# Kernel optimization log

Measured on AMD Instinct MI355X. Metric: run time of the kernel, lower is better.

The kernel has to match this reference:

```python
import jax, jax.numpy as jnp
import numpy as np

N_HEADS = 16
D_EMBED = 1024
D_HEAD = D_EMBED // N_HEADS
CAUSAL = False


def setup_inputs() -> dict:
    key = jax.random.key(0)
    k1, k2, k3, k4, k5 = jax.random.split(key, 5)
    B, S, D = 4, 2048, D_EMBED
    scale = 1.0 / np.sqrt(D)
    return {
        "x": jax.random.normal(k1, (B, S, D), dtype=jnp.float32),
        "w_in": jax.random.normal(k2, (D, 3 * D), dtype=jnp.float32) * scale,
        "b_in": jax.random.normal(k3, (3 * D,), dtype=jnp.float32) * 0.02,
        "w_out": jax.random.normal(k4, (D, D), dtype=jnp.float32) * scale,
        "b_out": jax.random.normal(k5, (D,), dtype=jnp.float32) * 0.02,
    }


def reference(x, w_in, b_in, w_out, b_out):
    B, S, D = x.shape
    qkv = jnp.einsum("bsd,de->bse", x, w_in) + b_in  # [B,S,3D]
    q, k, v = jnp.split(qkv, 3, axis=-1)
    # split heads -> [B,H,S,Dh]
    def sh(t):
        return t.reshape(B, S, N_HEADS, D_HEAD).transpose(0, 2, 1, 3)
    q, k, v = sh(q), sh(k), sh(v)
    weight = jnp.einsum("bhsd,bhtd->bhst", q, k)  # [B,H,S,S]
    if CAUSAL:
        mask = jnp.triu(jnp.ones((S, S), dtype=bool), k=1)
        weight = jnp.where(mask, -jnp.inf, weight)
    weight = weight / np.sqrt(D_HEAD)
    weight = jax.nn.softmax(weight, axis=-1)
    out = jnp.einsum("bhst,bhtd->bhsd", weight, v)
    out = out.transpose(0, 2, 1, 3).reshape(B, S, D)
    return jnp.einsum("bsd,de->bse", out, w_out) + b_out
```

## Files before the change

kernel.cpp:

```cpp
#include <hip/hip_runtime.h>
#include <hip/hip_bf16.h>

typedef unsigned short u16;
typedef __attribute__((ext_vector_type(8))) short bf16x8;
typedef __attribute__((ext_vector_type(4))) float f32x4;
typedef __attribute__((ext_vector_type(16))) float f32x16;

#define QSCALE 0.180336880f

#define DEV static __device__ __forceinline__

DEV u16 f2bf(float f) {
  union { float f; unsigned u; } v; v.f = f;
  unsigned r = v.u + 0x7fffu + ((v.u >> 16) & 1u);
  return (u16)(r >> 16);
}

DEV unsigned pk2(float a, float b) {
  union { __hip_bfloat162 h; unsigned u; } c;
  c.h = __float22bfloat162_rn(make_float2(a, b));
  return c.u;
}

DEV void gll16(void* lds, const void* g) {
  __builtin_amdgcn_global_load_lds(
      (const __attribute__((address_space(1))) unsigned int*)g,
      (__attribute__((address_space(3))) unsigned int*)lds, 16, 0, 0);
}

__global__ __launch_bounds__(256) void cvt_f32_to_bf16(const float* __restrict__ in,
                                                       u16* __restrict__ out, int n4) {
  int i = blockIdx.x * blockDim.x + threadIdx.x;
  int stride = gridDim.x * blockDim.x;
  for (; i < n4; i += stride) {
    float4 f = ((const float4*)in)[i];
    ushort4 u;
    u.x = f2bf(f.x); u.y = f2bf(f.y); u.z = f2bf(f.z); u.w = f2bf(f.w);
    ((ushort4*)out)[i] = u;
  }
}

__global__ __launch_bounds__(256) void transpose_cvt(const float* __restrict__ W,
                                                     u16* __restrict__ Wt,
                                                     int K, int N, int sn, float sval) {
  __shared__ u16 t[64][65];
  const int k0 = blockIdx.x * 64, n0 = blockIdx.y * 64;
  const int tid = threadIdx.x;
  const int rr = tid >> 4;
  const int cc = (tid & 15) * 4;
  const float scl = (n0 < sn) ? sval : 1.0f;
#pragma unroll
  for (int i = 0; i < 4; ++i) {
    const int row = rr * 4 + i;
    float4 f = *(const float4*)&W[(size_t)(k0 + row) * N + n0 + cc];
    t[row][cc + 0] = f2bf(f.x * scl);
    t[row][cc + 1] = f2bf(f.y * scl);
    t[row][cc + 2] = f2bf(f.z * scl);
    t[row][cc + 3] = f2bf(f.w * scl);
  }
  __syncthreads();
#pragma unroll
  for (int i = 0; i < 4; ++i) {
    const int n = rr * 4 + i;
    ushort4 u;
    u.x = t[cc + 0][n]; u.y = t[cc + 1][n]; u.z = t[cc + 2][n]; u.w = t[cc + 3][n];
    *(ushort4*)&Wt[(size_t)(n0 + n) * K + k0 + cc] = u;
  }
}

__global__ __launch_bounds__(256) void transpose_v(const u16* __restrict__ qkv,
                                                   u16* __restrict__ vT) {
  __shared__ u16 t[64][72];
  const int bh = blockIdx.y;
  const int b = bh >> 4, h = bh & 15;
  const int t0 = blockIdx.x * 64;
  const int tid = threadIdx.x;
  const int row = tid >> 2;
  const int cg = (tid & 3) * 16;
  const size_t src = (size_t)b * 2048 * 3072 + (size_t)(t0 + row) * 3072 + 2048 + h * 64 + cg;
  bf16x8 v0 = *(const bf16x8*)&qkv[src];
  bf16x8 v1 = *(const bf16x8*)&qkv[src + 8];
#pragma unroll
  for (int i = 0; i < 8; ++i) { t[row][cg + i] = (u16)v0[i]; t[row][cg + 8 + i] = (u16)v1[i]; }
  __syncthreads();
  const int d = tid >> 2;
  const int tg = (tid & 3) * 16;
  bf16x8 o0, o1;
#pragma unroll
  for (int i = 0; i < 8; ++i) { o0[i] = (short)t[tg + i][d]; o1[i] = (short)t[tg + 8 + i][d]; }
  u16* dst = &vT[((size_t)bh * 64 + d) * 2048 + t0 + tg];
  *(bf16x8*)dst = o0;
  *(bf16x8*)(dst + 8) = o1;
}

template<bool OUT_BF16>
__global__ __launch_bounds__(256) void gemm_bf16(const u16* __restrict__ A,
                                                 const u16* __restrict__ Bt,
                                                 const float* __restrict__ bias,
                                                 void* __restrict__ Cout,
                                                 int M, int N, int K, int qn,
                                                 u16* __restrict__ vTout, int vn0) {
  __shared__ __align__(16) u16 As[128][64];
  __shared__ __align__(16) u16 Bs[128][64];
  const int tid = threadIdx.x;
  const int wave = tid >> 6, lane = tid & 63;
  const int g = lane >> 4, lr = lane & 15;
  const int bm = blockIdx.x * 128, bn = blockIdx.y * 128;
  const int wm = (wave >> 1) * 64, wn = (wave & 1) * 64;
  f32x4 acc[4][4] = {};
  for (int kt = 0; kt < K; kt += 64) {
    __syncthreads();
#pragma unroll
    for (int j = 0; j < 4; ++j) {
      int chunk = wave * 4 + j;
      int e = chunk * 512 + lane * 8;
      int r = e >> 6, c = e & 63;
      gll16((u16*)As + chunk * 512, &A[(size_t)(bm + r) * K + kt + c]);
      gll16((u16*)Bs + chunk * 512, &Bt[(size_t)(bn + r) * K + kt + c]);
    }
    __syncthreads();
#pragma unroll
    for (int kk = 0; kk < 64; kk += 32) {
      bf16x8 af[4], bfr[4];
#pragma unroll
      for (int m = 0; m < 4; ++m)
        af[m] = *(const bf16x8*)&As[wm + m * 16 + lr][kk + g * 8];
#pragma unroll
      for (int n = 0; n < 4; ++n)
        bfr[n] = *(const bf16x8*)&Bs[wn + n * 16 + lr][kk + g * 8];
#pragma unroll
      for (int m = 0; m < 4; ++m)
#pragma unroll
        for (int n = 0; n < 4; ++n)
          acc[m][n] = __builtin_amdgcn_mfma_f32_16x16x32_bf16(af[m], bfr[n], acc[m][n], 0, 0, 0);
    }
  }
#pragma unroll
  for (int m = 0; m < 4; ++m) {
#pragma unroll
    for (int n = 0; n < 4; ++n) {
      const int col = bn + wn + n * 16 + lr;
      float bv = bias ? bias[col] : 0.f;
      if (col < qn) bv *= QSCALE;
      if (vTout != nullptr && col >= vn0) {
        const int hc = col - vn0;
#pragma unroll
        for (int r = 0; r < 4; ++r) {
          const int row = bm + wm + m * 16 + g * 4 + r;
          const size_t idx = (((size_t)(row >> 11) * 16 + (hc >> 6)) * 64 + (hc & 63)) * 2048
                             + (row & 2047);
          vTout[idx] = f2bf(acc[m][n][r] + bv);
        }
      } else {
#pragma unroll
        for (int r = 0; r < 4; ++r) {
          const int row = bm + wm + m * 16 + g * 4 + r;
          float v = acc[m][n][r] + bv;
          if (OUT_BF16) ((u16*)Cout)[(size_t)row * N + col] = f2bf(v);
          else          ((float*)Cout)[(size_t)row * N + col] = v;
        }
      }
    }
  }
}


#define ATTN_BODY(BUF, ISSUE, VM)                                                 \
  {                                                                               \
    if (ISSUE) {                                                                  \
      gll16((u16*)Ks[((BUF) + 2) & 3] + wave * 512, gk); gk += 32 * 3072;         \
      gll16((u16*)Vs[((BUF) + 2) & 3] + wave * 512, gv); gv += 32;                \
    }                                                                             \
    asm volatile("s_waitcnt vmcnt(" #VM ")" ::: "memory");                        \
    __builtin_amdgcn_s_barrier();                                                 \
    const char* kb = (const char*)Ks[(BUF)];                                      \
    const char* vb = (const char*)Vs[(BUF)];                                      \
    f32x16 s = {};                                                                \
    __builtin_amdgcn_s_setprio(1);                                                \
    _Pragma("unroll")                                                             \
    for (int kk = 0; kk < 4; ++kk) {                                              \
      bf16x8 kf = *(const bf16x8*)(kb + koff[kk]);                                \
      s = __builtin_amdgcn_mfma_f32_32x32x16_bf16(kf, qf[kk], s, 0, 0, 0);        \
    }                                                                             \
    __builtin_amdgcn_s_setprio(0);                                                \
    float pr[16];                                                                 \
    _Pragma("unroll")                                                             \
    for (int r = 0; r < 16; ++r) pr[r] = __builtin_amdgcn_exp2f(s[r]);            \
    lsum += ((pr[0] + pr[1]) + (pr[2] + pr[3])) + ((pr[4] + pr[5]) + (pr[6] + pr[7])) \
          + ((pr[8] + pr[9]) + (pr[10] + pr[11])) + ((pr[12] + pr[13]) + (pr[14] + pr[15])); \
    union { unsigned u[4]; bf16x8 v; } pa0, pa1;                                  \
    {                                                                             \
      unsigned X0 = pk2(pr[0], pr[1]), X1 = pk2(pr[2], pr[3]);                    \
      unsigned Y0 = pk2(pr[4], pr[5]), Y1 = pk2(pr[6], pr[7]);                    \
      asm volatile("v_permlane32_swap_b32 %0, %1" : "+v"(X0), "+v"(Y0));          \
      asm volatile("v_permlane32_swap_b32 %0, %1" : "+v"(X1), "+v"(Y1));          \
      pa0.u[0] = X0; pa0.u[1] = X1; pa0.u[2] = Y0; pa0.u[3] = Y1;                 \
      unsigned Z0 = pk2(pr[8], pr[9]), Z1 = pk2(pr[10], pr[11]);                  \
      unsigned W0 = pk2(pr[12], pr[13]), W1 = pk2(pr[14], pr[15]);                \
      asm volatile("v_permlane32_swap_b32 %0, %1" : "+v"(Z0), "+v"(W0));          \
      asm volatile("v_permlane32_swap_b32 %0, %1" : "+v"(Z1), "+v"(W1));          \
      pa1.u[0] = Z0; pa1.u[1] = Z1; pa1.u[2] = W0; pa1.u[3] = W1;                 \
    }                                                                             \
    __builtin_amdgcn_s_setprio(1);                                                \
    {                                                                             \
      bf16x8 vf00 = *(const bf16x8*)(vb + voff[0][0]);                            \
      bf16x8 vf10 = *(const bf16x8*)(vb + voff[1][0]);                            \
      o0 = __builtin_amdgcn_mfma_f32_32x32x16_bf16(pa0.v, vf00, o0, 0, 0, 0);     \
      o1 = __builtin_amdgcn_mfma_f32_32x32x16_bf16(pa0.v, vf10, o1, 0, 0, 0);     \
      bf16x8 vf01 = *(const bf16x8*)(vb + voff[0][1]);                            \
      bf16x8 vf11 = *(const bf16x8*)(vb + voff[1][1]);                            \
      o0 = __builtin_amdgcn_mfma_f32_32x32x16_bf16(pa1.v, vf01, o0, 0, 0, 0);     \
      o1 = __builtin_amdgcn_mfma_f32_32x32x16_bf16(pa1.v, vf11, o1, 0, 0, 0);     \
    }                                                                             \
    __builtin_amdgcn_s_setprio(0);                                                \
  }

__global__ __launch_bounds__(256, 4) void attn_kernel(const u16* __restrict__ qkv,
                                                      const u16* __restrict__ vT,
                                                      u16* __restrict__ out) {
  __shared__ __align__(16) u16 Ks[4][2048];
  __shared__ __align__(16) u16 Vs[4][2048];
  const int tid = threadIdx.x;
  const int wave = tid >> 6, lane = tid & 63;
  const int hi = lane >> 5, l31 = lane & 31;
  const int id = blockIdx.x;
  const int bh = ((id >> 3) & 7) * 8 + (id & 7);
  const int b = bh >> 4, h = bh & 15;
  const int q0 = (id >> 6) * 128;
  const size_t base = (size_t)b * 2048 * 3072;
  const u16* kg = qkv + base + 1024 + h * 64;
  const u16* vg = vT + (size_t)bh * 64 * 2048;

  const int qrow = q0 + wave * 32 + l31;
  bf16x8 qf[4];
#pragma unroll
  for (int kk = 0; kk < 4; ++kk)
    qf[kk] = *(const bf16x8*)&qkv[base + (size_t)qrow * 3072 + h * 64 + kk * 16 + hi * 8];

  int koff[4];
#pragma unroll
  for (int kk = 0; kk < 4; ++kk)
    koff[kk] = (kk * 2 + hi) * 512 + l31 * 16;
  int voff[2][2];
#pragma unroll
  for (int dt = 0; dt < 2; ++dt)
#pragma unroll
    for (int kp = 0; kp < 2; ++kp)
      voff[dt][kp] = (dt * 4 + kp * 2 + hi) * 512 + l31 * 16;

  const u16* gk = kg + (size_t)l31 * 3072 + wave * 16 + hi * 8;
  const u16* gv = vg + (size_t)((wave >> 1) * 32 + l31) * 2048 + (wave & 1) * 16 + hi * 8;

  f32x16 o0 = {}, o1 = {};
  float lsum = 0.f;

  gll16((u16*)Ks[0] + wave * 512, gk); gk += 32 * 3072;
  gll16((u16*)Vs[0] + wave * 512, gv); gv += 32;
  gll16((u16*)Ks[1] + wave * 512, gk); gk += 32 * 3072;
  gll16((u16*)Vs[1] + wave * 512, gv); gv += 32;

  for (int it4 = 0; it4 < 15; ++it4) {
    ATTN_BODY(0, true, 4)
    ATTN_BODY(1, true, 4)
    ATTN_BODY(2, true, 4)
    ATTN_BODY(3, true, 4)
  }
  ATTN_BODY(0, true, 4)
  ATTN_BODY(1, true, 4)
  ATTN_BODY(2, false, 2)
  ATTN_BODY(3, false, 0)

  float lt = lsum + __shfl_xor(lsum, 32);
  const size_t orow0 = (size_t)b * 2048 + q0 + wave * 32;
#pragma unroll
  for (int r = 0; r < 16; ++r) {
    const int crow = (r & 3) + 8 * (r >> 2) + 4 * hi;
    const float li = __shfl(lt, crow);
    u16* orow = out + (orow0 + crow) * 1024 + h * 64 + l31;
    orow[0]  = f2bf(o0[r] / li);
    orow[32] = f2bf(o1[r] / li);
  }
}

extern "C" void kernel_launch(void* const* d_in, const int* in_sizes, int n_in,
                              void* d_out, int out_size, void* d_ws, size_t ws_size,
                              hipStream_t stream) {
  (void)in_sizes; (void)n_in; (void)out_size;
  const float* x     = (const float*)d_in[0];
  const float* w_in  = (const float*)d_in[1];
  const float* b_in  = (const float*)d_in[2];
  const float* w_out = (const float*)d_in[3];
  const float* b_out = (const float*)d_in[4];
  float* out = (float*)d_out;

  char* ws = (char*)d_ws;
  u16* Xbf   = (u16*)ws; ws += (size_t)8192 * 1024 * 2;
  u16* WinT  = (u16*)ws; ws += (size_t)3072 * 1024 * 2;
  u16* WoutT = (u16*)ws; ws += (size_t)1024 * 1024 * 2;
  u16* qkv   = (u16*)ws; ws += (size_t)8192 * 3072 * 2;
  u16* attno = (u16*)ws; ws += (size_t)8192 * 1024 * 2;
  u16* vTsep = (u16*)ws;

  const size_t fused_need = 92274688ull + 16777216ull;
  const bool fused = (ws_size >= fused_need);
  u16* vT = fused ? vTsep : Xbf;

  cvt_f32_to_bf16<<<2048, 256, 0, stream>>>(x, Xbf, 8192 * 1024 / 4);
  transpose_cvt<<<dim3(16, 48), 256, 0, stream>>>(w_in, WinT, 1024, 3072, 1024, QSCALE);
  transpose_cvt<<<dim3(16, 16), 256, 0, stream>>>(w_out, WoutT, 1024, 1024, 0, 1.0f);
  if (fused) {
    gemm_bf16<true ><<<dim3(64, 24), 256, 0, stream>>>(Xbf, WinT, b_in, qkv,
                                                       8192, 3072, 1024, 1024, vT, 2048);
  } else {
    gemm_bf16<true ><<<dim3(64, 24), 256, 0, stream>>>(Xbf, WinT, b_in, qkv,
                                                       8192, 3072, 1024, 1024, nullptr, 1 << 30);
    transpose_v<<<dim3(32, 64), 256, 0, stream>>>(qkv, vT);
  }
  attn_kernel<<<1024, 256, 0, stream>>>(qkv, vT, attno);
  gemm_bf16<false><<<dim3(64, 8), 256, 0, stream>>>(attno, WoutT, b_out, out,
                                                    8192, 1024, 1024, 0, nullptr, 1 << 30);
}
```

Baseline: 226.6 us.

## Store V transposed inside QKV buffer, process 64-key tiles, XCD-aware GEMM tile mapping

The QKV GEMM epilogue now writes V in transposed layout into the unused V columns of the qkv buffer, so the separate vT workspace and the fallback transpose kernel go away. The attention loop moves from a 4-deep pipeline of 32-key tiles to a double-buffered loop over 64-key tiles, with two independent QK^T accumulators per step and one wait and barrier per tile. The GEMM block index is remapped so consecutive blocks on each XCD share A row tiles, aiming at better L2 reuse. In exchange, prefetch depth is shallower, register pressure per step is higher, and the V transposed-in-place indexing is intricate.

```diff
diff --git a/kernel.cpp b/kernel.cpp
--- a/kernel.cpp
+++ b/kernel.cpp
@@ -68,55 +68,33 @@
   }
 }
 
-__global__ __launch_bounds__(256) void transpose_v(const u16* __restrict__ qkv,
-                                                   u16* __restrict__ vT) {
-  __shared__ u16 t[64][72];
-  const int bh = blockIdx.y;
-  const int b = bh >> 4, h = bh & 15;
-  const int t0 = blockIdx.x * 64;
-  const int tid = threadIdx.x;
-  const int row = tid >> 2;
-  const int cg = (tid & 3) * 16;
-  const size_t src = (size_t)b * 2048 * 3072 + (size_t)(t0 + row) * 3072 + 2048 + h * 64 + cg;
-  bf16x8 v0 = *(const bf16x8*)&qkv[src];
-  bf16x8 v1 = *(const bf16x8*)&qkv[src + 8];
-#pragma unroll
-  for (int i = 0; i < 8; ++i) { t[row][cg + i] = (u16)v0[i]; t[row][cg + 8 + i] = (u16)v1[i]; }
-  __syncthreads();
-  const int d = tid >> 2;
-  const int tg = (tid & 3) * 16;
-  bf16x8 o0, o1;
-#pragma unroll
-  for (int i = 0; i < 8; ++i) { o0[i] = (short)t[tg + i][d]; o1[i] = (short)t[tg + 8 + i][d]; }
-  u16* dst = &vT[((size_t)bh * 64 + d) * 2048 + t0 + tg];
-  *(bf16x8*)dst = o0;
-  *(bf16x8*)(dst + 8) = o1;
-}
-
 template<bool OUT_BF16>
 __global__ __launch_bounds__(256) void gemm_bf16(const u16* __restrict__ A,
                                                  const u16* __restrict__ Bt,
                                                  const float* __restrict__ bias,
                                                  void* __restrict__ Cout,
-                                                 int M, int N, int K, int qn,
-                                                 u16* __restrict__ vTout, int vn0) {
+                                                 int M, int N, int K, int qn, int vn0) {
   __shared__ __align__(16) u16 As[128][64];
   __shared__ __align__(16) u16 Bs[128][64];
   const int tid = threadIdx.x;
   const int wave = tid >> 6, lane = tid & 63;
   const int g = lane >> 4, lr = lane & 15;
-  const int bm = blockIdx.x * 128, bn = blockIdx.y * 128;
+  const int lid = blockIdx.y * gridDim.x + blockIdx.x;
+  const int chunk = gridDim.x >> 3;
+  const int xcd = lid & 7, j = lid >> 3;
+  const int bm = (xcd * chunk + (j % chunk)) * 128;
+  const int bn = (j / chunk) * 128;
   const int wm = (wave >> 1) * 64, wn = (wave & 1) * 64;
   f32x4 acc[4][4] = {};
   for (int kt = 0; kt < K; kt += 64) {
     __syncthreads();
 #pragma unroll
-    for (int j = 0; j < 4; ++j) {
-      int chunk = wave * 4 + j;
-      int e = chunk * 512 + lane * 8;
+    for (int jj = 0; jj < 4; ++jj) {
+      int chnk = wave * 4 + jj;
+      int e = chnk * 512 + lane * 8;
       int r = e >> 6, c = e & 63;
-      gll16((u16*)As + chunk * 512, &A[(size_t)(bm + r) * K + kt + c]);
-      gll16((u16*)Bs + chunk * 512, &Bt[(size_t)(bn + r) * K + kt + c]);
+      gll16((u16*)As + chnk * 512, &A[(size_t)(bm + r) * K + kt + c]);
+      gll16((u16*)Bs + chnk * 512, &Bt[(size_t)(bn + r) * K + kt + c]);
     }
     __syncthreads();
 #pragma unroll
@@ -142,14 +120,15 @@
       const int col = bn + wn + n * 16 + lr;
       float bv = bias ? bias[col] : 0.f;
       if (col < qn) bv *= QSCALE;
-      if (vTout != nullptr && col >= vn0) {
+      if (col >= vn0) {
         const int hc = col - vn0;
 #pragma unroll
         for (int r = 0; r < 4; ++r) {
           const int row = bm + wm + m * 16 + g * 4 + r;
-          const size_t idx = (((size_t)(row >> 11) * 16 + (hc >> 6)) * 64 + (hc & 63)) * 2048
-                             + (row & 2047);
-          vTout[idx] = f2bf(acc[m][n][r] + bv);
+          const int t = row & 2047, bb = row >> 11;
+          const size_t idx = (size_t)bb * 6291456
+                           + ((size_t)hc * 2 + (t >> 10)) * 3072 + 2048 + (t & 1023);
+          ((u16*)Cout)[idx] = f2bf(acc[m][n][r] + bv);
         }
       } else {
 #pragma unroll
@@ -165,61 +144,94 @@
 }
 
 
-#define ATTN_BODY(BUF, ISSUE, VM)                                                 \
+#define ATTN_SUB(SOFF, PA0, PA1)                                                  \
+    f32x16 s##PA0 = {};                                                           \
+    (void)0
+
+#define ATTN_BODY(BUF, ISSUE)                                                     \
   {                                                                               \
     if (ISSUE) {                                                                  \
-      gll16((u16*)Ks[((BUF) + 2) & 3] + wave * 512, gk); gk += 32 * 3072;         \
-      gll16((u16*)Vs[((BUF) + 2) & 3] + wave * 512, gv); gv += 32;                \
-    }                                                                             \
-    asm volatile("s_waitcnt vmcnt(" #VM ")" ::: "memory");                        \
-    __builtin_amdgcn_s_barrier();                                                 \
+      gll16((u16*)Ks[(BUF) ^ 1] + wave * 512, gk);                                \
+      gll16((u16*)Ks[(BUF) ^ 1] + 2048 + wave * 512, gk + 32 * 3072);             \
+      gk += (size_t)64 * 3072;                                                    \
+      gll16((u16*)Vs[(BUF) ^ 1] + wave * 512, gv);                                \
+      gll16((u16*)Vs[(BUF) ^ 1] + 2048 + wave * 512, gv + 32);                    \
+      gv += 64;                                                                   \
+    }                                                                             \
     const char* kb = (const char*)Ks[(BUF)];                                      \
     const char* vb = (const char*)Vs[(BUF)];                                      \
-    f32x16 s = {};                                                                \
+    f32x16 sA = {}, sB = {};                                                      \
     __builtin_amdgcn_s_setprio(1);                                                \
     _Pragma("unroll")                                                             \
     for (int kk = 0; kk < 4; ++kk) {                                              \
-      bf16x8 kf = *(const bf16x8*)(kb + koff[kk]);                                \
-      s = __builtin_amdgcn_mfma_f32_32x32x16_bf16(kf, qf[kk], s, 0, 0, 0);        \
+      bf16x8 kfA = *(const bf16x8*)(kb + koff[kk]);                               \
+      bf16x8 kfB = *(const bf16x8*)(kb + 4096 + koff[kk]);                        \
+      sA = __builtin_amdgcn_mfma_f32_32x32x16_bf16(kfA, qf[kk], sA, 0, 0, 0);     \
+      sB = __builtin_amdgcn_mfma_f32_32x32x16_bf16(kfB, qf[kk], sB, 0, 0, 0);     \
     }                                                                             \
     __builtin_amdgcn_s_setprio(0);                                                \
-    float pr[16];                                                                 \
+    float prA[16], prB[16];                                                       \
     _Pragma("unroll")                                                             \
-    for (int r = 0; r < 16; ++r) pr[r] = __builtin_amdgcn_exp2f(s[r]);            \
-    lsum += ((pr[0] + pr[1]) + (pr[2] + pr[3])) + ((pr[4] + pr[5]) + (pr[6] + pr[7])) \
-          + ((pr[8] + pr[9]) + (pr[10] + pr[11])) + ((pr[12] + pr[13]) + (pr[14] + pr[15])); \
-    union { unsigned u[4]; bf16x8 v; } pa0, pa1;                                  \
+    for (int r = 0; r < 16; ++r) prA[r] = __builtin_amdgcn_exp2f(sA[r]);          \
+    _Pragma("unroll")                                                             \
+    for (int r = 0; r < 16; ++r) prB[r] = __builtin_amdgcn_exp2f(sB[r]);          \
+    lsum += (((prA[0] + prA[1]) + (prA[2] + prA[3])) + ((prA[4] + prA[5]) + (prA[6] + prA[7])))   \
+          + (((prA[8] + prA[9]) + (prA[10] + prA[11])) + ((prA[12] + prA[13]) + (prA[14] + prA[15]))); \
+    lsum += (((prB[0] + prB[1]) + (prB[2] + prB[3])) + ((prB[4] + prB[5]) + (prB[6] + prB[7])))   \
+          + (((prB[8] + prB[9]) + (prB[10] + prB[11])) + ((prB[12] + prB[13]) + (prB[14] + prB[15]))); \
+    union { unsigned u[4]; bf16x8 v; } pa0A, pa1A, pa0B, pa1B;                    \
     {                                                                             \
-      unsigned X0 = pk2(pr[0], pr[1]), X1 = pk2(pr[2], pr[3]);                    \
-      unsigned Y0 = pk2(pr[4], pr[5]), Y1 = pk2(pr[6], pr[7]);                    \
+      unsigned X0 = pk2(prA[0], prA[1]), X1 = pk2(prA[2], prA[3]);                \
+      unsigned Y0 = pk2(prA[4], prA[5]), Y1 = pk2(prA[6], prA[7]);                \
       asm volatile("v_permlane32_swap_b32 %0, %1" : "+v"(X0), "+v"(Y0));          \
       asm volatile("v_permlane32_swap_b32 %0, %1" : "+v"(X1), "+v"(Y1));          \
-      pa0.u[0] = X0; pa0.u[1] = X1; pa0.u[2] = Y0; pa0.u[3] = Y1;                 \
-      unsigned Z0 = pk2(pr[8], pr[9]), Z1 = pk2(pr[10], pr[11]);                  \
-      unsigned W0 = pk2(pr[12], pr[13]), W1 = pk2(pr[14], pr[15]);                \
+      pa0A.u[0] = X0; pa0A.u[1] = X1; pa0A.u[2] = Y0; pa0A.u[3] = Y1;             \
+      unsigned Z0 = pk2(prA[8], prA[9]), Z1 = pk2(prA[10], prA[11]);              \
+      unsigned W0 = pk2(prA[12], prA[13]), W1 = pk2(prA[14], prA[15]);            \
       asm volatile("v_permlane32_swap_b32 %0, %1" : "+v"(Z0), "+v"(W0));          \
       asm volatile("v_permlane32_swap_b32 %0, %1" : "+v"(Z1), "+v"(W1));          \
-      pa1.u[0] = Z0; pa1.u[1] = Z1; pa1.u[2] = W0; pa1.u[3] = W1;                 \
+      pa1A.u[0] = Z0; pa1A.u[1] = Z1; pa1A.u[2] = W0; pa1A.u[3] = W1;             \
+    }                                                                             \
+    {                                                                             \
+      unsigned X0 = pk2(prB[0], prB[1]), X1 = pk2(prB[2], prB[3]);                \
+      unsigned Y0 = pk2(prB[4], prB[5]), Y1 = pk2(prB[6], prB[7]);                \
+      asm volatile("v_permlane32_swap_b32 %0, %1" : "+v"(X0), "+v"(Y0));          \
+      asm volatile("v_permlane32_swap_b32 %0, %1" : "+v"(X1), "+v"(Y1));          \
+      pa0B.u[0] = X0; pa0B.u[1] = X1; pa0B.u[2] = Y0; pa0B.u[3] = Y1;             \
+      unsigned Z0 = pk2(prB[8], prB[9]), Z1 = pk2(prB[10], prB[11]);              \
+      unsigned W0 = pk2(prB[12], prB[13]), W1 = pk2(prB[14], prB[15]);            \
+      asm volatile("v_permlane32_swap_b32 %0, %1" : "+v"(Z0), "+v"(W0));          \
+      asm volatile("v_permlane32_swap_b32 %0, %1" : "+v"(Z1), "+v"(W1));          \
+      pa1B.u[0] = Z0; pa1B.u[1] = Z1; pa1B.u[2] = W0; pa1B.u[3] = W1;             \
     }                                                                             \
     __builtin_amdgcn_s_setprio(1);                                                \
     {                                                                             \
-      bf16x8 vf00 = *(const bf16x8*)(vb + voff[0][0]);                            \
-      bf16x8 vf10 = *(const bf16x8*)(vb + voff[1][0]);                            \
-      o0 = __builtin_amdgcn_mfma_f32_32x32x16_bf16(pa0.v, vf00, o0, 0, 0, 0);     \
-      o1 = __builtin_amdgcn_mfma_f32_32x32x16_bf16(pa0.v, vf10, o1, 0, 0, 0);     \
-      bf16x8 vf01 = *(const bf16x8*)(vb + voff[0][1]);                            \
-      bf16x8 vf11 = *(const bf16x8*)(vb + voff[1][1]);                            \
-      o0 = __builtin_amdgcn_mfma_f32_32x32x16_bf16(pa1.v, vf01, o0, 0, 0, 0);     \
-      o1 = __builtin_amdgcn_mfma_f32_32x32x16_bf16(pa1.v, vf11, o1, 0, 0, 0);     \
+      bf16x8 vfA00 = *(const bf16x8*)(vb + voff[0][0]);                           \
+      bf16x8 vfA10 = *(const bf16x8*)(vb + voff[1][0]);                           \
+      o0 = __builtin_amdgcn_mfma_f32_32x32x16_bf16(pa0A.v, vfA00, o0, 0, 0, 0);   \
+      o1 = __builtin_amdgcn_mfma_f32_32x32x16_bf16(pa0A.v, vfA10, o1, 0, 0, 0);   \
+      bf16x8 vfA01 = *(const bf16x8*)(vb + voff[0][1]);                           \
+      bf16x8 vfA11 = *(const bf16x8*)(vb + voff[1][1]);                           \
+      o0 = __builtin_amdgcn_mfma_f32_32x32x16_bf16(pa1A.v, vfA01, o0, 0, 0, 0);   \
+      o1 = __builtin_amdgcn_mfma_f32_32x32x16_bf16(pa1A.v, vfA11, o1, 0, 0, 0);   \
+      bf16x8 vfB00 = *(const bf16x8*)(vb + 4096 + voff[0][0]);                    \
+      bf16x8 vfB10 = *(const bf16x8*)(vb + 4096 + voff[1][0]);                    \
+      o0 = __builtin_amdgcn_mfma_f32_32x32x16_bf16(pa0B.v, vfB00, o0, 0, 0, 0);   \
+      o1 = __builtin_amdgcn_mfma_f32_32x32x16_bf16(pa0B.v, vfB10, o1, 0, 0, 0);   \
+      bf16x8 vfB01 = *(const bf16x8*)(vb + 4096 + voff[0][1]);                    \
+      bf16x8 vfB11 = *(const bf16x8*)(vb + 4096 + voff[1][1]);                    \
+      o0 = __builtin_amdgcn_mfma_f32_32x32x16_bf16(pa1B.v, vfB01, o0, 0, 0, 0);   \
+      o1 = __builtin_amdgcn_mfma_f32_32x32x16_bf16(pa1B.v, vfB11, o1, 0, 0, 0);   \
     }                                                                             \
     __builtin_amdgcn_s_setprio(0);                                                \
+    asm volatile("s_waitcnt vmcnt(0)" ::: "memory");                              \
+    __builtin_amdgcn_s_barrier();                                                 \
   }
 
 __global__ __launch_bounds__(256, 4) void attn_kernel(const u16* __restrict__ qkv,
-                                                      const u16* __restrict__ vT,
                                                       u16* __restrict__ out) {
-  __shared__ __align__(16) u16 Ks[4][2048];
-  __shared__ __align__(16) u16 Vs[4][2048];
+  __shared__ __align__(16) u16 Ks[2][4096];
+  __shared__ __align__(16) u16 Vs[2][4096];
   const int tid = threadIdx.x;
   const int wave = tid >> 6, lane = tid & 63;
   const int hi = lane >> 5, l31 = lane & 31;
@@ -229,7 +241,6 @@
   const int q0 = (id >> 6) * 128;
   const size_t base = (size_t)b * 2048 * 3072;
   const u16* kg = qkv + base + 1024 + h * 64;
-  const u16* vg = vT + (size_t)bh * 64 * 2048;
 
   const int qrow = q0 + wave * 32 + l31;
   bf16x8 qf[4];
@@ -249,26 +260,28 @@
       voff[dt][kp] = (dt * 4 + kp * 2 + hi) * 512 + l31 * 16;
 
   const u16* gk = kg + (size_t)l31 * 3072 + wave * 16 + hi * 8;
-  const u16* gv = vg + (size_t)((wave >> 1) * 32 + l31) * 2048 + (wave & 1) * 16 + hi * 8;
+  const u16* gv = qkv + base + 2048 + (size_t)(h * 64 + (wave >> 1) * 32 + l31) * 6144
+                + (wave & 1) * 16 + hi * 8;
 
   f32x16 o0 = {}, o1 = {};
   float lsum = 0.f;
 
-  gll16((u16*)Ks[0] + wave * 512, gk); gk += 32 * 3072;
-  gll16((u16*)Vs[0] + wave * 512, gv); gv += 32;
-  gll16((u16*)Ks[1] + wave * 512, gk); gk += 32 * 3072;
-  gll16((u16*)Vs[1] + wave * 512, gv); gv += 32;
-
-  for (int it4 = 0; it4 < 15; ++it4) {
-    ATTN_BODY(0, true, 4)
-    ATTN_BODY(1, true, 4)
-    ATTN_BODY(2, true, 4)
-    ATTN_BODY(3, true, 4)
-  }
-  ATTN_BODY(0, true, 4)
-  ATTN_BODY(1, true, 4)
-  ATTN_BODY(2, false, 2)
-  ATTN_BODY(3, false, 0)
+  gll16((u16*)Ks[0] + wave * 512, gk);
+  gll16((u16*)Ks[0] + 2048 + wave * 512, gk + 32 * 3072);
+  gk += (size_t)64 * 3072;
+  gll16((u16*)Vs[0] + wave * 512, gv);
+  gll16((u16*)Vs[0] + 2048 + wave * 512, gv + 32);
+  gv += 64;
+  asm volatile("s_waitcnt vmcnt(0)" ::: "memory");
+  __builtin_amdgcn_s_barrier();
+
+  for (int it = 0; it < 7; ++it) { ATTN_BODY(0, true) ATTN_BODY(1, true) }
+  ATTN_BODY(0, true)
+  gv += 2048;
+  ATTN_BODY(1, true)
+  for (int it = 0; it < 7; ++it) { ATTN_BODY(0, true) ATTN_BODY(1, true) }
+  ATTN_BODY(0, true)
+  ATTN_BODY(1, false)
 
   float lt = lsum + __shfl_xor(lsum, 32);
   const size_t orow0 = (size_t)b * 2048 + q0 + wave * 32;
@@ -285,7 +298,7 @@
 extern "C" void kernel_launch(void* const* d_in, const int* in_sizes, int n_in,
                               void* d_out, int out_size, void* d_ws, size_t ws_size,
                               hipStream_t stream) {
-  (void)in_sizes; (void)n_in; (void)out_size;
+  (void)in_sizes; (void)n_in; (void)out_size; (void)ws_size;
   const float* x     = (const float*)d_in[0];
   const float* w_in  = (const float*)d_in[1];
   const float* b_in  = (const float*)d_in[2];
@@ -298,25 +311,14 @@
   u16* WinT  = (u16*)ws; ws += (size_t)3072 * 1024 * 2;
   u16* WoutT = (u16*)ws; ws += (size_t)1024 * 1024 * 2;
   u16* qkv   = (u16*)ws; ws += (size_t)8192 * 3072 * 2;
-  u16* attno = (u16*)ws; ws += (size_t)8192 * 1024 * 2;
-  u16* vTsep = (u16*)ws;
-
-  const size_t fused_need = 92274688ull + 16777216ull;
-  const bool fused = (ws_size >= fused_need);
-  u16* vT = fused ? vTsep : Xbf;
+  u16* attno = (u16*)ws;
 
   cvt_f32_to_bf16<<<2048, 256, 0, stream>>>(x, Xbf, 8192 * 1024 / 4);
   transpose_cvt<<<dim3(16, 48), 256, 0, stream>>>(w_in, WinT, 1024, 3072, 1024, QSCALE);
   transpose_cvt<<<dim3(16, 16), 256, 0, stream>>>(w_out, WoutT, 1024, 1024, 0, 1.0f);
-  if (fused) {
-    gemm_bf16<true ><<<dim3(64, 24), 256, 0, stream>>>(Xbf, WinT, b_in, qkv,
-                                                       8192, 3072, 1024, 1024, vT, 2048);
-  } else {
-    gemm_bf16<true ><<<dim3(64, 24), 256, 0, stream>>>(Xbf, WinT, b_in, qkv,
-                                                       8192, 3072, 1024, 1024, nullptr, 1 << 30);
-    transpose_v<<<dim3(32, 64), 256, 0, stream>>>(qkv, vT);
-  }
-  attn_kernel<<<1024, 256, 0, stream>>>(qkv, vT, attno);
+  gemm_bf16<true ><<<dim3(64, 24), 256, 0, stream>>>(Xbf, WinT, b_in, qkv,
+                                                     8192, 3072, 1024, 1024, 2048);
+  attn_kernel<<<1024, 256, 0, stream>>>(qkv, attno);
   gemm_bf16<false><<<dim3(64, 8), 256, 0, stream>>>(attno, WoutT, b_out, out,
-                                                    8192, 1024, 1024, 0, nullptr, 1 << 30);
-}
+                                                    8192, 1024, 1024, 0, 1 << 30);
+}
```

After: 261.5 us. 1.15x slower.

## Double-buffer 64-key attention tiles, swizzle GEMM blocks by XCD, drop fused V transpose

Applied to the files above, without the earlier changes.

The attention loop moves from four 32-key LDS buffers with partial vmcnt waits to two 64-key buffers. Each buffer is processed as two subtiles, followed by a full wait and a barrier, which halves the number of barriers per key. The GEMM remaps block indices so that each XCD gets a contiguous band of M tiles, aiming for better L2 reuse. The fused V-transpose epilogue, with its scattered 2-byte stores, is dropped in favour of always running the separate transpose_v kernel. That adds a launch and an extra pass over V, and the full vmcnt(0) wait each iteration may expose more load latency.

```diff
diff --git a/kernel.cpp b/kernel.cpp
--- a/kernel.cpp
+++ b/kernel.cpp
@@ -26,6 +26,21 @@
   __builtin_amdgcn_global_load_lds(
       (const __attribute__((address_space(1))) unsigned int*)g,
       (__attribute__((address_space(3))) unsigned int*)lds, 16, 0, 0);
+}
+
+DEV void packP(const float* pr, bf16x8* a0, bf16x8* a1) {
+  unsigned X0 = pk2(pr[0], pr[1]), X1 = pk2(pr[2], pr[3]);
+  unsigned Y0 = pk2(pr[4], pr[5]), Y1 = pk2(pr[6], pr[7]);
+  asm volatile("v_permlane32_swap_b32 %0, %1" : "+v"(X0), "+v"(Y0));
+  asm volatile("v_permlane32_swap_b32 %0, %1" : "+v"(X1), "+v"(Y1));
+  union { unsigned u[4]; bf16x8 v; } c0, c1;
+  c0.u[0] = X0; c0.u[1] = X1; c0.u[2] = Y0; c0.u[3] = Y1;
+  unsigned Z0 = pk2(pr[8], pr[9]), Z1 = pk2(pr[10], pr[11]);
+  unsigned W0 = pk2(pr[12], pr[13]), W1 = pk2(pr[14], pr[15]);
+  asm volatile("v_permlane32_swap_b32 %0, %1" : "+v"(Z0), "+v"(W0));
+  asm volatile("v_permlane32_swap_b32 %0, %1" : "+v"(Z1), "+v"(W1));
+  c1.u[0] = Z0; c1.u[1] = Z1; c1.u[2] = W0; c1.u[3] = W1;
+  *a0 = c0.v; *a1 = c1.v;
 }
 
 __global__ __launch_bounds__(256) void cvt_f32_to_bf16(const float* __restrict__ in,
@@ -98,25 +113,28 @@
                                                  const u16* __restrict__ Bt,
                                                  const float* __restrict__ bias,
                                                  void* __restrict__ Cout,
-                                                 int M, int N, int K, int qn,
-                                                 u16* __restrict__ vTout, int vn0) {
+                                                 int M, int N, int K, int qn) {
   __shared__ __align__(16) u16 As[128][64];
   __shared__ __align__(16) u16 Bs[128][64];
   const int tid = threadIdx.x;
   const int wave = tid >> 6, lane = tid & 63;
   const int g = lane >> 4, lr = lane & 15;
-  const int bm = blockIdx.x * 128, bn = blockIdx.y * 128;
+  const int lid = blockIdx.y * gridDim.x + blockIdx.x;
+  const int chunk = gridDim.x >> 3;
+  const int xcd = lid & 7, j = lid >> 3;
+  const int bm = (xcd * chunk + (j % chunk)) * 128;
+  const int bn = (j / chunk) * 128;
   const int wm = (wave >> 1) * 64, wn = (wave & 1) * 64;
   f32x4 acc[4][4] = {};
   for (int kt = 0; kt < K; kt += 64) {
     __syncthreads();
 #pragma unroll
-    for (int j = 0; j < 4; ++j) {
-      int chunk = wave * 4 + j;
-      int e = chunk * 512 + lane * 8;
+    for (int jj = 0; jj < 4; ++jj) {
+      int chnk = wave * 4 + jj;
+      int e = chnk * 512 + lane * 8;
       int r = e >> 6, c = e & 63;
-      gll16((u16*)As + chunk * 512, &A[(size_t)(bm + r) * K + kt + c]);
-      gll16((u16*)Bs + chunk * 512, &Bt[(size_t)(bn + r) * K + kt + c]);
+      gll16((u16*)As + chnk * 512, &A[(size_t)(bm + r) * K + kt + c]);
+      gll16((u16*)Bs + chnk * 512, &Bt[(size_t)(bn + r) * K + kt + c]);
     }
     __syncthreads();
 #pragma unroll
@@ -142,84 +160,72 @@
       const int col = bn + wn + n * 16 + lr;
       float bv = bias ? bias[col] : 0.f;
       if (col < qn) bv *= QSCALE;
-      if (vTout != nullptr && col >= vn0) {
-        const int hc = col - vn0;
-#pragma unroll
-        for (int r = 0; r < 4; ++r) {
-          const int row = bm + wm + m * 16 + g * 4 + r;
-          const size_t idx = (((size_t)(row >> 11) * 16 + (hc >> 6)) * 64 + (hc & 63)) * 2048
-                             + (row & 2047);
-          vTout[idx] = f2bf(acc[m][n][r] + bv);
-        }
-      } else {
-#pragma unroll
-        for (int r = 0; r < 4; ++r) {
-          const int row = bm + wm + m * 16 + g * 4 + r;
-          float v = acc[m][n][r] + bv;
-          if (OUT_BF16) ((u16*)Cout)[(size_t)row * N + col] = f2bf(v);
-          else          ((float*)Cout)[(size_t)row * N + col] = v;
-        }
+#pragma unroll
+      for (int r = 0; r < 4; ++r) {
+        const int row = bm + wm + m * 16 + g * 4 + r;
+        float v = acc[m][n][r] + bv;
+        if (OUT_BF16) ((u16*)Cout)[(size_t)row * N + col] = f2bf(v);
+        else          ((float*)Cout)[(size_t)row * N + col] = v;
       }
     }
   }
 }
 
 
-#define ATTN_BODY(BUF, ISSUE, VM)                                                 \
+#define ATTN_SUBTILE(KB, VB)                                                      \
   {                                                                               \
-    if (ISSUE) {                                                                  \
-      gll16((u16*)Ks[((BUF) + 2) & 3] + wave * 512, gk); gk += 32 * 3072;         \
-      gll16((u16*)Vs[((BUF) + 2) & 3] + wave * 512, gv); gv += 32;                \
-    }                                                                             \
-    asm volatile("s_waitcnt vmcnt(" #VM ")" ::: "memory");                        \
-    __builtin_amdgcn_s_barrier();                                                 \
-    const char* kb = (const char*)Ks[(BUF)];                                      \
-    const char* vb = (const char*)Vs[(BUF)];                                      \
     f32x16 s = {};                                                                \
     __builtin_amdgcn_s_setprio(1);                                                \
     _Pragma("unroll")                                                             \
     for (int kk = 0; kk < 4; ++kk) {                                              \
-      bf16x8 kf = *(const bf16x8*)(kb + koff[kk]);                                \
+      bf16x8 kf = *(const bf16x8*)((KB) + koff[kk]);                              \
       s = __builtin_amdgcn_mfma_f32_32x32x16_bf16(kf, qf[kk], s, 0, 0, 0);        \
     }                                                                             \
     __builtin_amdgcn_s_setprio(0);                                                \
     float pr[16];                                                                 \
     _Pragma("unroll")                                                             \
     for (int r = 0; r < 16; ++r) pr[r] = __builtin_amdgcn_exp2f(s[r]);            \
-    lsum += ((pr[0] + pr[1]) + (pr[2] + pr[3])) + ((pr[4] + pr[5]) + (pr[6] + pr[7])) \
-          + ((pr[8] + pr[9]) + (pr[10] + pr[11])) + ((pr[12] + pr[13]) + (pr[14] + pr[15])); \
-    union { unsigned u[4]; bf16x8 v; } pa0, pa1;                                  \
-    {                                                                             \
-      unsigned X0 = pk2(pr[0], pr[1]), X1 = pk2(pr[2], pr[3]);                    \
-      unsigned Y0 = pk2(pr[4], pr[5]), Y1 = pk2(pr[6], pr[7]);                    \
-      asm volatile("v_permlane32_swap_b32 %0, %1" : "+v"(X0), "+v"(Y0));          \
-      asm volatile("v_permlane32_swap_b32 %0, %1" : "+v"(X1), "+v"(Y1));          \
-      pa0.u[0] = X0; pa0.u[1] = X1; pa0.u[2] = Y0; pa0.u[3] = Y1;                 \
-      unsigned Z0 = pk2(pr[8], pr[9]), Z1 = pk2(pr[10], pr[11]);                  \
-      unsigned W0 = pk2(pr[12], pr[13]), W1 = pk2(pr[14], pr[15]);                \
-      asm volatile("v_permlane32_swap_b32 %0, %1" : "+v"(Z0), "+v"(W0));          \
-      asm volatile("v_permlane32_swap_b32 %0, %1" : "+v"(Z1), "+v"(W1));          \
-      pa1.u[0] = Z0; pa1.u[1] = Z1; pa1.u[2] = W0; pa1.u[3] = W1;                 \
-    }                                                                             \
+    lsum += (((pr[0] + pr[1]) + (pr[2] + pr[3])) + ((pr[4] + pr[5]) + (pr[6] + pr[7])))  \
+          + (((pr[8] + pr[9]) + (pr[10] + pr[11])) + ((pr[12] + pr[13]) + (pr[14] + pr[15]))); \
+    bf16x8 pa0, pa1;                                                              \
+    packP(pr, &pa0, &pa1);                                                        \
     __builtin_amdgcn_s_setprio(1);                                                \
     {                                                                             \
-      bf16x8 vf00 = *(const bf16x8*)(vb + voff[0][0]);                            \
-      bf16x8 vf10 = *(const bf16x8*)(vb + voff[1][0]);                            \
-      o0 = __builtin_amdgcn_mfma_f32_32x32x16_bf16(pa0.v, vf00, o0, 0, 0, 0);     \
-      o1 = __builtin_amdgcn_mfma_f32_32x32x16_bf16(pa0.v, vf10, o1, 0, 0, 0);     \
-      bf16x8 vf01 = *(const bf16x8*)(vb + voff[0][1]);                            \
-      bf16x8 vf11 = *(const bf16x8*)(vb + voff[1][1]);                            \
-      o0 = __builtin_amdgcn_mfma_f32_32x32x16_bf16(pa1.v, vf01, o0, 0, 0, 0);     \
-      o1 = __builtin_amdgcn_mfma_f32_32x32x16_bf16(pa1.v, vf11, o1, 0, 0, 0);     \
+      bf16x8 vf00 = *(const bf16x8*)((VB) + voff[0][0]);                          \
+      bf16x8 vf10 = *(const bf16x8*)((VB) + voff[1][0]);                          \
+      o0 = __builtin_amdgcn_mfma_f32_32x32x16_bf16(pa0, vf00, o0, 0, 0, 0);       \
+      o1 = __builtin_amdgcn_mfma_f32_32x32x16_bf16(pa0, vf10, o1, 0, 0, 0);       \
+      bf16x8 vf01 = *(const bf16x8*)((VB) + voff[0][1]);                          \
+      bf16x8 vf11 = *(const bf16x8*)((VB) + voff[1][1]);                          \
+      o0 = __builtin_amdgcn_mfma_f32_32x32x16_bf16(pa1, vf01, o0, 0, 0, 0);       \
+      o1 = __builtin_amdgcn_mfma_f32_32x32x16_bf16(pa1, vf11, o1, 0, 0, 0);       \
     }                                                                             \
     __builtin_amdgcn_s_setprio(0);                                                \
+  }
+
+#define ATTN_BODY(BUF, ISSUE)                                                     \
+  {                                                                               \
+    if (ISSUE) {                                                                  \
+      gll16((u16*)Ks[(BUF) ^ 1] + wave * 512, gk);                                \
+      gll16((u16*)Ks[(BUF) ^ 1] + 2048 + wave * 512, gk + 32 * 3072);             \
+      gk += (size_t)64 * 3072;                                                    \
+      gll16((u16*)Vs[(BUF) ^ 1] + wave * 512, gv);                                \
+      gll16((u16*)Vs[(BUF) ^ 1] + 2048 + wave * 512, gv + 32);                    \
+      gv += 64;                                                                   \
+    }                                                                             \
+    const char* kb = (const char*)Ks[(BUF)];                                      \
+    const char* vb = (const char*)Vs[(BUF)];                                      \
+    ATTN_SUBTILE(kb, vb)                                                          \
+    ATTN_SUBTILE(kb + 4096, vb + 4096)                                            \
+    asm volatile("s_waitcnt vmcnt(0)" ::: "memory");                              \
+    __builtin_amdgcn_s_barrier();                                                 \
   }
 
 __global__ __launch_bounds__(256, 4) void attn_kernel(const u16* __restrict__ qkv,
                                                       const u16* __restrict__ vT,
                                                       u16* __restrict__ out) {
-  __shared__ __align__(16) u16 Ks[4][2048];
-  __shared__ __align__(16) u16 Vs[4][2048];
+  __shared__ __align__(16) u16 Ks[2][4096];
+  __shared__ __align__(16) u16 Vs[2][4096];
   const int tid = threadIdx.x;
   const int wave = tid >> 6, lane = tid & 63;
   const int hi = lane >> 5, l31 = lane & 31;
@@ -254,21 +260,18 @@
   f32x16 o0 = {}, o1 = {};
   float lsum = 0.f;
 
-  gll16((u16*)Ks[0] + wave * 512, gk); gk += 32 * 3072;
-  gll16((u16*)Vs[0] + wave * 512, gv); gv += 32;
-  gll16((u16*)Ks[1] + wave * 512, gk); gk += 32 * 3072;
-  gll16((u16*)Vs[1] + wave * 512, gv); gv += 32;
-
-  for (int it4 = 0; it4 < 15; ++it4) {
-    ATTN_BODY(0, true, 4)
-    ATTN_BODY(1, true, 4)
-    ATTN_BODY(2, true, 4)
-    ATTN_BODY(3, true, 4)
-  }
-  ATTN_BODY(0, true, 4)
-  ATTN_BODY(1, true, 4)
-  ATTN_BODY(2, false, 2)
-  ATTN_BODY(3, false, 0)
+  gll16((u16*)Ks[0] + wave * 512, gk);
+  gll16((u16*)Ks[0] + 2048 + wave * 512, gk + 32 * 3072);
+  gk += (size_t)64 * 3072;
+  gll16((u16*)Vs[0] + wave * 512, gv);
+  gll16((u16*)Vs[0] + 2048 + wave * 512, gv + 32);
+  gv += 64;
+  asm volatile("s_waitcnt vmcnt(0)" ::: "memory");
+  __builtin_amdgcn_s_barrier();
+
+  for (int it = 0; it < 15; ++it) { ATTN_BODY(0, true) ATTN_BODY(1, true) }
+  ATTN_BODY(0, true)
+  ATTN_BODY(1, false)
 
   float lt = lsum + __shfl_xor(lsum, 32);
   const size_t orow0 = (size_t)b * 2048 + q0 + wave * 32;
@@ -285,7 +288,7 @@
 extern "C" void kernel_launch(void* const* d_in, const int* in_sizes, int n_in,
                               void* d_out, int out_size, void* d_ws, size_t ws_size,
                               hipStream_t stream) {
-  (void)in_sizes; (void)n_in; (void)out_size;
+  (void)in_sizes; (void)n_in; (void)out_size; (void)ws_size;
   const float* x     = (const float*)d_in[0];
   const float* w_in  = (const float*)d_in[1];
   const float* b_in  = (const float*)d_in[2];
@@ -298,25 +301,14 @@
   u16* WinT  = (u16*)ws; ws += (size_t)3072 * 1024 * 2;
   u16* WoutT = (u16*)ws; ws += (size_t)1024 * 1024 * 2;
   u16* qkv   = (u16*)ws; ws += (size_t)8192 * 3072 * 2;
-  u16* attno = (u16*)ws; ws += (size_t)8192 * 1024 * 2;
-  u16* vTsep = (u16*)ws;
-
-  const size_t fused_need = 92274688ull + 16777216ull;
-  const bool fused = (ws_size >= fused_need);
-  u16* vT = fused ? vTsep : Xbf;
+  u16* attno = (u16*)ws;
+  u16* vT    = Xbf;
 
   cvt_f32_to_bf16<<<2048, 256, 0, stream>>>(x, Xbf, 8192 * 1024 / 4);
   transpose_cvt<<<dim3(16, 48), 256, 0, stream>>>(w_in, WinT, 1024, 3072, 1024, QSCALE);
   transpose_cvt<<<dim3(16, 16), 256, 0, stream>>>(w_out, WoutT, 1024, 1024, 0, 1.0f);
-  if (fused) {
-    gemm_bf16<true ><<<dim3(64, 24), 256, 0, stream>>>(Xbf, WinT, b_in, qkv,
-                                                       8192, 3072, 1024, 1024, vT, 2048);
-  } else {
-    gemm_bf16<true ><<<dim3(64, 24), 256, 0, stream>>>(Xbf, WinT, b_in, qkv,
-                                                       8192, 3072, 1024, 1024, nullptr, 1 << 30);
-    transpose_v<<<dim3(32, 64), 256, 0, stream>>>(qkv, vT);
-  }
+  gemm_bf16<true ><<<dim3(64, 24), 256, 0, stream>>>(Xbf, WinT, b_in, qkv, 8192, 3072, 1024, 1024);
+  transpose_v<<<dim3(32, 64), 256, 0, stream>>>(qkv, vT);
   attn_kernel<<<1024, 256, 0, stream>>>(qkv, vT, attno);
-  gemm_bf16<false><<<dim3(64, 8), 256, 0, stream>>>(attno, WoutT, b_out, out,
-                                                    8192, 1024, 1024, 0, nullptr, 1 << 30);
-}
+  gemm_bf16<false><<<dim3(64, 8), 256, 0, stream>>>(attno, WoutT, b_out, out, 8192, 1024, 1024, 0);
+}
```

New measurement: 251.1 us. +10.8%, slower.

## Add 256x256 pipelined QKV GEMM kernel with XCD-aware tile mapping

Applied to the files above, without the earlier changes.

Replaces the 128x128 QKV projection GEMM with a new 512-thread kernel that computes 256x256 tiles. It uses a 4-stage LDS ring with async global-to-LDS loads, vmcnt-based waits and raised wave priority around the MFMA block. Blocks are remapped so consecutive M tiles land on the same XCD, and the output-projection GEMM gets the same remapping. The fused V-transpose epilogue is dropped in favour of always running the separate transpose_v kernel, which adds one extra pass over V in exchange for simpler, coalesced GEMM stores.

```diff
diff --git a/kernel.cpp b/kernel.cpp
--- a/kernel.cpp
+++ b/kernel.cpp
@@ -93,30 +93,125 @@
   *(bf16x8*)(dst + 8) = o1;
 }
 
+
+#define G1_STAGE(S)                                                   \
+  {                                                                   \
+    gll16((u16*)L1[S] + wave * 512, g0); g0 += 32;                    \
+    gll16((u16*)L1[S] + 4096 + wave * 512, g1); g1 += 32;             \
+    gll16((u16*)L1[S] + 8192 + wave * 512, g2); g2 += 32;             \
+    gll16((u16*)L1[S] + 12288 + wave * 512, g3); g3 += 32;            \
+  }
+
+#define G1_BODY(S, ISSUE, VM)                                         \
+  {                                                                   \
+    if (ISSUE) G1_STAGE((S + 2) & 3)                                  \
+    asm volatile("s_waitcnt vmcnt(" #VM ")" ::: "memory");            \
+    __builtin_amdgcn_s_barrier();                                     \
+    const char* sb = (const char*)L1[S];                              \
+    bf16x8 af[8], bfr[4];                                             \
+    _Pragma("unroll")                                                 \
+    for (int m = 0; m < 8; ++m) af[m] = *(const bf16x8*)(sb + aoff[m]); \
+    _Pragma("unroll")                                                 \
+    for (int n = 0; n < 4; ++n) bfr[n] = *(const bf16x8*)(sb + boff[n]); \
+    __builtin_amdgcn_s_setprio(1);                                    \
+    _Pragma("unroll")                                                 \
+    for (int m = 0; m < 8; ++m)                                       \
+      _Pragma("unroll")                                               \
+      for (int n = 0; n < 4; ++n)                                     \
+        acc[m][n] = __builtin_amdgcn_mfma_f32_16x16x32_bf16(af[m], bfr[n], acc[m][n], 0, 0, 0); \
+    __builtin_amdgcn_s_setprio(0);                                    \
+  }
+
+__global__ __launch_bounds__(512, 2) void gemm1_256(const u16* __restrict__ A,
+                                                    const u16* __restrict__ Bt,
+                                                    const float* __restrict__ bias,
+                                                    u16* __restrict__ C) {
+  __shared__ __align__(16) u16 L1[4][16384];
+  const int tid = threadIdx.x;
+  const int wave = tid >> 6, lane = tid & 63;
+  const int g = lane >> 4, lr = lane & 15;
+  const int wr = wave >> 2, wc = wave & 3;
+  const int id = blockIdx.x;
+  const int xcd = id & 7, j = id >> 3;
+  const int bm = (xcd * 4 + (j & 3)) * 256;
+  const int bn = (j >> 2) * 256;
+
+  int aoff[8], boff[4];
+#pragma unroll
+  for (int m = 0; m < 8; ++m)
+    aoff[m] = wr * 8192 + m * 1024 + g * 256 + lr * 16;
+#pragma unroll
+  for (int n = 0; n < 4; ++n)
+    boff[n] = 16384 + wc * 4096 + n * 1024 + g * 256 + lr * 16;
+
+  const u16* g0; const u16* g1; const u16* g2; const u16* g3;
+  {
+    const int b0 = wave * 1024 + lane * 16;
+    const int plane = b0 >> 8, lrr = (b0 >> 4) & 15, pb = b0 & 15;
+    const int row = (plane >> 2) * 16 + lrr;
+    const int kc = (plane & 3) * 8 + (pb >> 1);
+    g0 = A  + (size_t)(bm + row) * 1024 + kc;
+    g1 = A  + (size_t)(bm + 128 + row) * 1024 + kc;
+    g2 = Bt + (size_t)(bn + row) * 1024 + kc;
+    g3 = Bt + (size_t)(bn + 128 + row) * 1024 + kc;
+  }
+
+  f32x4 acc[8][4] = {};
+
+  G1_STAGE(0)
+  G1_STAGE(1)
+
+  for (int it = 0; it < 7; ++it) {
+    G1_BODY(0, 1, 8) G1_BODY(1, 1, 8) G1_BODY(2, 1, 8) G1_BODY(3, 1, 8)
+  }
+  G1_BODY(0, 1, 8)
+  G1_BODY(1, 1, 8)
+  G1_BODY(2, 0, 4)
+  G1_BODY(3, 0, 0)
+
+#pragma unroll
+  for (int m = 0; m < 8; ++m) {
+#pragma unroll
+    for (int n = 0; n < 4; ++n) {
+      const int col = bn + wc * 64 + n * 16 + lr;
+      float bv = bias[col];
+      if (col < 1024) bv *= QSCALE;
+#pragma unroll
+      for (int r = 0; r < 4; ++r) {
+        const int row = bm + wr * 128 + m * 16 + g * 4 + r;
+        C[(size_t)row * 3072 + col] = f2bf(acc[m][n][r] + bv);
+      }
+    }
+  }
+}
+
 template<bool OUT_BF16>
 __global__ __launch_bounds__(256) void gemm_bf16(const u16* __restrict__ A,
                                                  const u16* __restrict__ Bt,
                                                  const float* __restrict__ bias,
                                                  void* __restrict__ Cout,
-                                                 int M, int N, int K, int qn,
-                                                 u16* __restrict__ vTout, int vn0) {
+                                                 int M, int N, int K, int qn) {
   __shared__ __align__(16) u16 As[128][64];
   __shared__ __align__(16) u16 Bs[128][64];
   const int tid = threadIdx.x;
   const int wave = tid >> 6, lane = tid & 63;
   const int g = lane >> 4, lr = lane & 15;
-  const int bm = blockIdx.x * 128, bn = blockIdx.y * 128;
+  const int lid = blockIdx.y * gridDim.x + blockIdx.x;
+  const int chunk = gridDim.x >> 3;
+  const int xcd = lid & 7, j = lid >> 3;
+  const int bm = (xcd * chunk + (j % chunk)) * 128;
+  const int bn = (j / chunk) * 128;
   const int wm = (wave >> 1) * 64, wn = (wave & 1) * 64;
   f32x4 acc[4][4] = {};
   for (int kt = 0; kt < K; kt += 64) {
     __syncthreads();
 #pragma unroll
-    for (int j = 0; j < 4; ++j) {
-      int chunk = wave * 4 + j;
-      int e = chunk * 512 + lane * 8;
+    for (int jj = 0; jj < 4; ++jj) {
+      int chnk = wave * 4 + jj;
+      int e = chnk * 512 + lane * 8;
       int r = e >> 6, c = e & 63;
-      gll16((u16*)As + chunk * 512, &A[(size_t)(bm + r) * K + kt + c]);
-      gll16((u16*)Bs + chunk * 512, &Bt[(size_t)(bn + r) * K + kt + c]);
+      gll16((u16*)As + chnk * 512, &A[(size_t)(bm + r) * K + kt + c]);
+      gll16((u16*)Bs + chnk * 512, &Bt[(size_t)(bn + r) * K + kt + c]);
     }
     __syncthreads();
 #pragma unroll
@@ -142,23 +237,12 @@
       const int col = bn + wn + n * 16 + lr;
       float bv = bias ? bias[col] : 0.f;
       if (col < qn) bv *= QSCALE;
-      if (vTout != nullptr && col >= vn0) {
-        const int hc = col - vn0;
-#pragma unroll
-        for (int r = 0; r < 4; ++r) {
-          const int row = bm + wm + m * 16 + g * 4 + r;
-          const size_t idx = (((size_t)(row >> 11) * 16 + (hc >> 6)) * 64 + (hc & 63)) * 2048
-                             + (row & 2047);
-          vTout[idx] = f2bf(acc[m][n][r] + bv);
-        }
-      } else {
-#pragma unroll
-        for (int r = 0; r < 4; ++r) {
-          const int row = bm + wm + m * 16 + g * 4 + r;
-          float v = acc[m][n][r] + bv;
-          if (OUT_BF16) ((u16*)Cout)[(size_t)row * N + col] = f2bf(v);
-          else          ((float*)Cout)[(size_t)row * N + col] = v;
-        }
+#pragma unroll
+      for (int r = 0; r < 4; ++r) {
+        const int row = bm + wm + m * 16 + g * 4 + r;
+        float v = acc[m][n][r] + bv;
+        if (OUT_BF16) ((u16*)Cout)[(size_t)row * N + col] = f2bf(v);
+        else          ((float*)Cout)[(size_t)row * N + col] = v;
       }
     }
   }
@@ -285,7 +369,7 @@
 extern "C" void kernel_launch(void* const* d_in, const int* in_sizes, int n_in,
                               void* d_out, int out_size, void* d_ws, size_t ws_size,
                               hipStream_t stream) {
-  (void)in_sizes; (void)n_in; (void)out_size;
+  (void)in_sizes; (void)n_in; (void)out_size; (void)ws_size;
   const float* x     = (const float*)d_in[0];
   const float* w_in  = (const float*)d_in[1];
   const float* b_in  = (const float*)d_in[2];
@@ -298,25 +382,14 @@
   u16* WinT  = (u16*)ws; ws += (size_t)3072 * 1024 * 2;
   u16* WoutT = (u16*)ws; ws += (size_t)1024 * 1024 * 2;
   u16* qkv   = (u16*)ws; ws += (size_t)8192 * 3072 * 2;
-  u16* attno = (u16*)ws; ws += (size_t)8192 * 1024 * 2;
-  u16* vTsep = (u16*)ws;
-
-  const size_t fused_need = 92274688ull + 16777216ull;
-  const bool fused = (ws_size >= fused_need);
-  u16* vT = fused ? vTsep : Xbf;
+  u16* attno = (u16*)ws;
+  u16* vT    = Xbf;
 
   cvt_f32_to_bf16<<<2048, 256, 0, stream>>>(x, Xbf, 8192 * 1024 / 4);
   transpose_cvt<<<dim3(16, 48), 256, 0, stream>>>(w_in, WinT, 1024, 3072, 1024, QSCALE);
   transpose_cvt<<<dim3(16, 16), 256, 0, stream>>>(w_out, WoutT, 1024, 1024, 0, 1.0f);
-  if (fused) {
-    gemm_bf16<true ><<<dim3(64, 24), 256, 0, stream>>>(Xbf, WinT, b_in, qkv,
-                                                       8192, 3072, 1024, 1024, vT, 2048);
-  } else {
-    gemm_bf16<true ><<<dim3(64, 24), 256, 0, stream>>>(Xbf, WinT, b_in, qkv,
-                                                       8192, 3072, 1024, 1024, nullptr, 1 << 30);
-    transpose_v<<<dim3(32, 64), 256, 0, stream>>>(qkv, vT);
-  }
+  gemm1_256<<<384, 512, 0, stream>>>(Xbf, WinT, b_in, qkv);
+  transpose_v<<<dim3(32, 64), 256, 0, stream>>>(qkv, vT);
   attn_kernel<<<1024, 256, 0, stream>>>(qkv, vT, attno);
-  gemm_bf16<false><<<dim3(64, 8), 256, 0, stream>>>(attno, WoutT, b_out, out,
-                                                    8192, 1024, 1024, 0, nullptr, 1 << 30);
-}
+  gemm_bf16<false><<<dim3(64, 8), 256, 0, stream>>>(attno, WoutT, b_out, out, 8192, 1024, 1024, 0);
+}
```

Result: no change. 223.3 us (-1.5%).
